# Kernel tuning notes

Hardware: AMD Instinct MI355X
Metric: run time of the kernel (lower is better)

The kernel has to match this reference:

```python
import jax, jax.numpy as jnp
import numpy as np

B, L, DIN = 2, 4096, 1024
W = 64            # windowsize
G, H = 8, 8       # groups, heads per group
DQ = DV = 64
FF = 1024
NEG = -1e30


def rmsnorm(x, gamma, d):
    # F.normalize(x, dim=-1) * sqrt(d) * gamma
    n = jnp.sqrt(jnp.sum(x * x, axis=-1, keepdims=True))
    return x / jnp.maximum(n, 1e-12) * (d ** 0.5) * gamma


def setup_inputs() -> dict:
    key = jax.random.key(0)
    ks = jax.random.split(key, 8)
    s = 0.02
    return {
        "x": jax.random.normal(ks[0], (B, L, DIN), jnp.float32),
        "norm_gamma": jnp.ones((DIN,), jnp.float32),
        "Wq_w": jax.random.normal(ks[1], (G * H * DQ, DIN), jnp.float32) * s,
        "Wq_b": jnp.zeros((G * H * DQ,), jnp.float32),
        "Wkv_w": jax.random.normal(ks[2], (G * (DQ + DV), DIN), jnp.float32) * s,
        "Wkv_b": jnp.zeros((G * (DQ + DV),), jnp.float32),
        "wz_gamma1": jnp.ones((G * H * DV,), jnp.float32),
        "W1_w": jax.random.normal(ks[3], (2 * FF, G * H * DV), jnp.float32) * s,
        "W1_b": jnp.zeros((2 * FF,), jnp.float32),
        "wz_gamma2": jnp.ones((2 * FF,), jnp.float32),
        "W2_w": jax.random.normal(ks[4], (FF, 2 * FF), jnp.float32) * s,
        "W2_b": jnp.zeros((FF,), jnp.float32),
    }


def reference(x, norm_gamma, Wq_w, Wq_b, Wkv_w, Wkv_b,
              wz_gamma1, W1_w, W1_b, wz_gamma2, W2_w, W2_b):
    w2, w4 = W // 2, W // 4
    S = 2 * L // W  # number of query chunks (L % W == 0 -> drop_last path)

    xn = rmsnorm(x, norm_gamma, DIN)
    q = xn @ Wq_w.T + Wq_b          # [B, L, G*H*DQ]
    kv = xn @ Wkv_w.T + Wkv_b       # [B, L, G*(DQ+DV)]

    # pad_to_multiple(kv, W, mod=W//2): L % W == 0 -> append W//2 zeros
    kv = jnp.pad(kv, ((0, 0), (0, w2), (0, 0)))
    k, v = jnp.split(kv, 2, axis=-1)  # each [B, L+W/2, G*DQ]
    # F.pad W//4 both sides, then overlapping windows of size W, stride W//2
    k = jnp.pad(k, ((0, 0), (w4, w4), (0, 0)))  # [B, L+W, G*DQ]
    v = jnp.pad(v, ((0, 0), (w4, w4), (0, 0)))
    idx = jnp.arange(S)[:, None] * w2 + jnp.arange(W)[None, :]  # [S, W] (drop_last applied)
    kwin = k[:, idx].reshape(B, S, W, G, DQ).transpose(0, 3, 1, 2, 4)  # [B,G,S,W,DQ]
    vwin = v[:, idx].reshape(B, S, W, G, DV).transpose(0, 3, 1, 2, 4)  # [B,G,S,W,DV]

    # 'B (S w) (G H D) -> B G H S w D'
    qh = q.reshape(B, S, w2, G, H, DQ).transpose(0, 3, 4, 1, 2, 5)  # [B,G,H,S,w2,DQ]

    qk = jnp.einsum('bghsqd,bgskd->bghsqk', qh, kwin) * (1.0 / DQ ** 0.5)
    # edge masking: first chunk can't see left pad, last chunk can't see right pad
    maskb = jnp.zeros((S, W), bool).at[0, :w4].set(True).at[S - 1, W - w4:].set(True)
    qk = jnp.where(maskb[None, None, None, :, None, :], NEG, qk)
    attn = jax.nn.softmax(qk, axis=-1)
    o = jnp.einsum('bghsqk,bgskd->bghsqd', attn, vwin)
    o = o.transpose(0, 3, 4, 1, 2, 5).reshape(B, L, G * H * DV)  # 'B G H S w D -> B (S w) (G H D)'

    # Wz: RMSNorm -> Linear -> SiLU -> RMSNorm -> Linear -> SiLU (dropout=0)
    z = rmsnorm(o, wz_gamma1, G * H * DV)
    z = jax.nn.silu(z @ W1_w.T + W1_b)
    z = rmsnorm(z, wz_gamma2, 2 * FF)
    z = jax.nn.silu(z @ W2_w.T + W2_b)
    return z
```

## Files before the change

### kernel.cpp

```cpp
#include <hip/hip_runtime.h>
#include <cstdint>

typedef _Float16 f16;
typedef f16 f16x4 __attribute__((ext_vector_type(4)));
typedef f16 f16x8 __attribute__((ext_vector_type(8)));
typedef float f32x4 __attribute__((ext_vector_type(4)));

#define MFMA16(a, b, c) __builtin_amdgcn_mfma_f32_16x16x32_f16(a, b, c, 0, 0, 0)

static __device__ __forceinline__ void gload16(const void* g, void* l) {
    __builtin_amdgcn_global_load_lds(
        (const __attribute__((address_space(1))) uint32_t*)g,
        (__attribute__((address_space(3))) uint32_t*)l, 16, 0, 0);
}

template <int NM, int ND, int NV>
static __device__ __forceinline__ void sgb_phase() {
    if (NV > 0) __builtin_amdgcn_sched_group_barrier(0x10, NV, 0);
    constexpr int PER = NM / ND;
#pragma unroll
    for (int i = 0; i < ND; ++i) {
        __builtin_amdgcn_sched_group_barrier(0x8, PER, 0);
        __builtin_amdgcn_sched_group_barrier(0x100, 1, 0);
    }
    if (NM - PER * ND > 0)
        __builtin_amdgcn_sched_group_barrier(0x8, NM - PER * ND, 0);
}

static __device__ __forceinline__ float blockReduceSum256(float v) {
    __shared__ float red[4];
#pragma unroll
    for (int off = 32; off > 0; off >>= 1) v += __shfl_xor(v, off);
    if ((threadIdx.x & 63) == 0) red[threadIdx.x >> 6] = v;
    __syncthreads();
    return red[0] + red[1] + red[2] + red[3];
}

template <int D>
__global__ __launch_bounds__(256) void k_rowss(const f16* __restrict__ in,
                                               float* __restrict__ sc) {
    constexpr int PER = D / 256;
    size_t row = blockIdx.x;
    const f16* ir = in + row * D;
    int c0 = threadIdx.x * PER;
    float ss = 0.f;
#pragma unroll
    for (int i = 0; i < PER; i += 8) {
        f16x8 h = *reinterpret_cast<const f16x8*>(ir + c0 + i);
#pragma unroll
        for (int e = 0; e < 8; ++e) { float f = (float)h[e]; ss += f * f; }
    }
    ss = blockReduceSum256(ss);
    if (threadIdx.x == 0) sc[row] = ss;
}

__global__ __launch_bounds__(256) void k_prep(
    const float* __restrict__ x, const float* __restrict__ ng, f16* __restrict__ xn,
    const float* __restrict__ Wq_w, const float* __restrict__ Wkv_w,
    const float* __restrict__ W1_w, const float* __restrict__ g1,
    const float* __restrict__ W2_w, const float* __restrict__ g2,
    const float* __restrict__ Wq_b, const float* __restrict__ Wkv_b,
    f16* __restrict__ wqkv, f16* __restrict__ w1, f16* __restrict__ w2,
    float* __restrict__ cb, float* __restrict__ scz) {
    if (blockIdx.x < 8192) {
        size_t row = blockIdx.x;
        const float4 v = reinterpret_cast<const float4*>(x + row * 1024)[threadIdx.x];
        float ss = v.x * v.x + v.y * v.y + v.z * v.z + v.w * v.w;
        ss = blockReduceSum256(ss);
        float sc = 32.0f / fmaxf(sqrtf(ss), 1e-12f);
        const float4 g = reinterpret_cast<const float4*>(ng)[threadIdx.x];
        f16x4 o;
        o[0] = (f16)(v.x * sc * g.x); o[1] = (f16)(v.y * sc * g.y);
        o[2] = (f16)(v.z * sc * g.z); o[3] = (f16)(v.w * sc * g.w);
        *reinterpret_cast<f16x4*>(xn + row * 1024 + threadIdx.x * 4) = o;
        return;
    }
    int i = (blockIdx.x - 8192) * 256 + threadIdx.x;
    if (i < 1048576) {
        float4 v = reinterpret_cast<const float4*>(Wq_w)[i];
        f16x4 o; o[0] = (f16)v.x; o[1] = (f16)v.y; o[2] = (f16)v.z; o[3] = (f16)v.w;
        *reinterpret_cast<f16x4*>(wqkv + (size_t)i * 4) = o;
    } else if (i < 1310720) {
        int j = i - 1048576;
        float4 v = reinterpret_cast<const float4*>(Wkv_w)[j];
        f16x4 o; o[0] = (f16)v.x; o[1] = (f16)v.y; o[2] = (f16)v.z; o[3] = (f16)v.w;
        *reinterpret_cast<f16x4*>(wqkv + 4194304 + (size_t)j * 4) = o;
    } else if (i < 3407872) {
        int j = i - 1310720;
        float4 v = reinterpret_cast<const float4*>(W1_w)[j];
        int c = (j * 4) & 4095;
        f16x4 o;
        o[0] = (f16)(v.x * g1[c]);     o[1] = (f16)(v.y * g1[c + 1]);
        o[2] = (f16)(v.z * g1[c + 2]); o[3] = (f16)(v.w * g1[c + 3]);
        *reinterpret_cast<f16x4*>(w1 + (size_t)j * 4) = o;
    } else if (i < 3932160) {
        int j = i - 3407872;
        float4 v = reinterpret_cast<const float4*>(W2_w)[j];
        int c = (j * 4) & 2047;
        f16x4 o;
        o[0] = (f16)(v.x * g2[c]);     o[1] = (f16)(v.y * g2[c + 1]);
        o[2] = (f16)(v.z * g2[c + 2]); o[3] = (f16)(v.w * g2[c + 3]);
        *reinterpret_cast<f16x4*>(w2 + (size_t)j * 4) = o;
    } else if (i < 3933440) {
        int j = i - 3932160;
        int e = j * 4;
        float4 o4 = (e < 4096) ? reinterpret_cast<const float4*>(Wq_b)[j]
                               : reinterpret_cast<const float4*>(Wkv_b)[(e - 4096) >> 2];
        reinterpret_cast<float4*>(cb)[j] = o4;
    } else if (i < 3937536) {
        int j = i - 3933440;
        reinterpret_cast<float4*>(scz)[j] = make_float4(0.f, 0.f, 0.f, 0.f);
    }
}

template <int BM, int BN, int EPI>
__global__ __launch_bounds__(512, 2) void k_gemm8p(const f16* __restrict__ A,
                                                   const f16* __restrict__ Bt,
                                                   const float* __restrict__ bias,
                                                   const float* __restrict__ ssin,
                                                   float sqrtD,
                                                   void* __restrict__ Cout,
                                                   int M, int N, int K) {
    constexpr int WN = BN / 64, WM = 8 / WN, WR = BM / WM;
    constexpr int MW = WR / 16, MH = MW / 2;
    constexpr int LA = BM / 128, LB = BN / 128;
    constexpr int VS = 2 * LA + LB;
    constexpr int AK = BM * 32;
    constexpr int BKE = BN * 32;
    constexpr int SE = 2 * AK + 2 * BKE;

    __shared__ alignas(16) f16 lds[2 * SE];

    const int mb = M / BM;
    const int cpx = mb >> 3;
    const int xcd = blockIdx.x & 7;
    const int j = blockIdx.x >> 3;
    const int bm = xcd * cpx + (j % cpx);
    const int bn = j / cpx;

    const int tid = threadIdx.x, w = tid >> 6, l = tid & 63;
    const int wm = w / WN, wn = w % WN;
    const int lrow = l & 15, lq = l >> 4;
    const int g = (lrow >> 1) & 3;

    const f16* Ab = A + (size_t)bm * BM * K;
    const f16* Bb = Bt + (size_t)bn * BN * K;
    const int NT = K >> 6;

    int aoff[MW], boff[4];
#pragma unroll
    for (int m = 0; m < MW; ++m)
        aoff[m] = (wm * WR + m * 16 + lrow) * 32 + 8 * (lq ^ g);
#pragma unroll
    for (int n = 0; n < 4; ++n)
        boff[n] = (wn * 64 + n * 16 + lrow) * 32 + 8 * (lq ^ g);

    auto stageA = [&](int k0, f16* region) {
#pragma unroll
        for (int q = 0; q < LA; ++q) {
            int r = q * 128 + w * 16 + (l >> 2);
            int c = 8 * ((l & 3) ^ ((r >> 1) & 3));
            gload16(Ab + (size_t)r * K + k0 + c, region + q * 4096 + w * 512);
        }
    };
    auto stageB = [&](int k0, f16* region) {
#pragma unroll
        for (int q = 0; q < LB; ++q) {
            int r = q * 128 + w * 16 + (l >> 2);
            int c = 8 * ((l & 3) ^ ((r >> 1) & 3));
            gload16(Bb + (size_t)r * K + k0 + c, region + q * 4096 + w * 512);
        }
    };
    auto rdA = [&](f16x8 (&d)[MH], const f16* base, int h) {
#pragma unroll
        for (int m = 0; m < MH; ++m)
            d[m] = *reinterpret_cast<const f16x8*>(base + aoff[h * MH + m]);
    };
    auto rdB = [&](f16x8 (&d)[4], const f16* base) {
#pragma unroll
        for (int n = 0; n < 4; ++n)
            d[n] = *reinterpret_cast<const f16x8*>(base + boff[n]);
    };

    f32x4 acc[MW][4] = {};
    f16x8 afA[MH], afB[MH], bfA[4], bfB[4];

    auto mfmaLo = [&](f16x8 (&af)[MH], f16x8 (&bf)[4]) {
        __builtin_amdgcn_s_setprio(1);
#pragma unroll
        for (int m = 0; m < MH; ++m)
#pragma unroll
            for (int n = 0; n < 4; ++n)
                acc[m][n] = MFMA16(af[m], bf[n], acc[m][n]);
        __builtin_amdgcn_s_setprio(0);
    };
    auto mfmaHi = [&](f16x8 (&af)[MH], f16x8 (&bf)[4]) {
        __builtin_amdgcn_s_setprio(1);
#pragma unroll
        for (int m = 0; m < MH; ++m)
#pragma unroll
            for (int n = 0; n < 4; ++n)
                acc[MH + m][n] = MFMA16(af[m], bf[n], acc[MH + m][n]);
        __builtin_amdgcn_s_setprio(0);
    };

    stageA(0, lds);             stageB(0, lds + 2 * AK);
    stageA(32, lds + AK);       stageB(32, lds + 2 * AK + BKE);
    stageA(64, lds + SE);       stageB(64, lds + SE + 2 * AK);
    asm volatile("s_waitcnt vmcnt(%0)" :: "i"(2 * (LA + LB)) : "memory");
    __builtin_amdgcn_s_barrier();
    rdA(afA, lds, 0);
    rdB(bfA, lds + 2 * AK);

    const int NTm2 = NT - 2;
    for (int t = 0; t < NTm2; ++t) {
        f16* s0 = lds + (t & 1) * SE;
        f16* s1 = lds + ((t & 1) ^ 1) * SE;
        const int kn1 = (t + 1) << 6;
        const int kn2 = (t + 2) << 6;
        __builtin_amdgcn_s_barrier();
        stageA(kn1 + 32, s1 + AK);
        rdA(afB, s0, 1);
        mfmaLo(afA, bfA);
        sgb_phase<MH * 4, MH, LA>();
        asm volatile("s_waitcnt vmcnt(%0)" :: "i"(VS) : "memory");
        __builtin_amdgcn_s_barrier();
        stageB(kn1 + 32, s1 + 2 * AK + BKE);
        rdA(afA, s0 + AK, 0);
        rdB(bfB, s0 + 2 * AK + BKE);
        mfmaHi(afB, bfA);
        sgb_phase<MH * 4, MH + 4, LB>();
        __builtin_amdgcn_s_barrier();
        stageA(kn2, s0);
        rdA(afB, s0 + AK, 1);
        mfmaLo(afA, bfB);
        sgb_phase<MH * 4, MH, LA>();
        asm volatile("s_waitcnt vmcnt(%0)" :: "i"(VS) : "memory");
        __builtin_amdgcn_s_barrier();
        stageB(kn2, s0 + 2 * AK);
        rdA(afA, s1, 0);
        rdB(bfA, s1 + 2 * AK);
        mfmaHi(afB, bfB);
        sgb_phase<MH * 4, MH + 4, LB>();
    }
    {
        const int t = NTm2;
        f16* s0 = lds + (t & 1) * SE;
        f16* s1 = lds + ((t & 1) ^ 1) * SE;
        const int kn1 = (t + 1) << 6;
        __builtin_amdgcn_s_barrier();
        stageA(kn1 + 32, s1 + AK);
        rdA(afB, s0, 1);
        mfmaLo(afA, bfA);
        sgb_phase<MH * 4, MH, LA>();
        asm volatile("s_waitcnt vmcnt(%0)" :: "i"(VS) : "memory");
        __builtin_amdgcn_s_barrier();
        stageB(kn1 + 32, s1 + 2 * AK + BKE);
        rdA(afA, s0 + AK, 0);
        rdB(bfB, s0 + 2 * AK + BKE);
        mfmaHi(afB, bfA);
        sgb_phase<MH * 4, MH + 4, LB>();
        __builtin_amdgcn_s_barrier();
        rdA(afB, s0 + AK, 1);
        mfmaLo(afA, bfB);
        sgb_phase<MH * 4, MH, 0>();
        asm volatile("s_waitcnt vmcnt(%0)" :: "i"(LA + LB) : "memory");
        __builtin_amdgcn_s_barrier();
        rdA(afA, s1, 0);
        rdB(bfA, s1 + 2 * AK);
        mfmaHi(afB, bfB);
        sgb_phase<MH * 4, MH + 4, 0>();
    }
    {
        f16* s0 = lds + ((NT - 1) & 1) * SE;
        __builtin_amdgcn_s_barrier();
        rdA(afB, s0, 1);
        mfmaLo(afA, bfA);
        sgb_phase<MH * 4, MH, 0>();
        asm volatile("s_waitcnt vmcnt(0)" ::: "memory");
        __builtin_amdgcn_s_barrier();
        rdA(afA, s0 + AK, 0);
        rdB(bfB, s0 + 2 * AK + BKE);
        mfmaHi(afB, bfA);
        sgb_phase<MH * 4, MH + 4, 0>();
        __builtin_amdgcn_s_barrier();
        rdA(afB, s0 + AK, 1);
        mfmaLo(afA, bfB);
        sgb_phase<MH * 4, MH, 0>();
        mfmaHi(afB, bfB);
    }

    const size_t row0 = (size_t)bm * BM + wm * WR;
    const int col0 = bn * BN + wn * 64;
    float bsv[4];
#pragma unroll
    for (int n = 0; n < 4; ++n) bsv[n] = bias[col0 + n * 16 + lrow];
#pragma unroll
    for (int m = 0; m < MW; ++m) {
#pragma unroll
        for (int r = 0; r < 4; ++r) {
            const size_t row = row0 + m * 16 + lq * 4 + r;
            float scl = 1.0f;
            if (EPI >= 1) scl = sqrtD * rsqrtf(fmaxf(ssin[row], 1e-24f));
#pragma unroll
            for (int n = 0; n < 4; ++n) {
                float v = acc[m][n][r];
                if (EPI >= 1) v = v * scl;
                v += bsv[n];
                if (EPI >= 1) v = v / (1.f + __expf(-v));
                const size_t idx = row * (size_t)N + col0 + n * 16 + lrow;
                if (EPI == 2) reinterpret_cast<float*>(Cout)[idx] = v;
                else          reinterpret_cast<f16*>(Cout)[idx] = (f16)v;
            }
        }
    }
}

__global__ __launch_bounds__(256) void k_attn(const f16* __restrict__ qkv,
                                              f16* __restrict__ o,
                                              float* __restrict__ ssout) {
    __shared__ alignas(16) f16 Ksm[64 * 64];
    __shared__ alignas(16) f16 Vtsm[64 * 64];
    __shared__ alignas(16) f16 Psm[4][64 * 64];
    const int idx = blockIdx.x;
    const int s = idx & 127;
    const int g = (idx >> 7) & 7;
    const int b = idx >> 10;
    const int tid = threadIdx.x;
    const int w = tid >> 6, l = tid & 63;

    const int baseR = s * 32 - 16;
#pragma unroll
    for (int i = 0; i < 2; ++i) {
        const int j = i * 32 + (tid >> 3);
        const int d0 = (tid & 7) * 8;
        const int R = baseR + j;
        f16x8 kvv = {}, vvv = {};
        if (R >= 0 && R < 4096) {
            const f16* rp = qkv + ((size_t)(b * 4096 + R)) * 5120 + 4096 + g * 64 + d0;
            kvv = *reinterpret_cast<const f16x8*>(rp);
            vvv = *reinterpret_cast<const f16x8*>(rp + 512);
        }
        *reinterpret_cast<f16x8*>(&Ksm[j * 64 + d0]) = kvv;
#pragma unroll
        for (int e = 0; e < 8; ++e) Vtsm[(d0 + e) * 64 + j] = vvv[e];
    }

    const int lrow = l & 15, lk = (l >> 4) * 8;
    f16x8 aq[4][2];
#pragma unroll
    for (int m = 0; m < 4; ++m) {
        const int qr = w * 64 + m * 16 + lrow;
        const int h = qr >> 5, qi = qr & 31;
        const f16* qp = qkv + ((size_t)(b * 4096 + s * 32 + qi)) * 5120 + (g * 8 + h) * 64 + lk;
        aq[m][0] = *reinterpret_cast<const f16x8*>(qp);
        aq[m][1] = *reinterpret_cast<const f16x8*>(qp + 32);
    }
    __syncthreads();

    f32x4 acc[4][4] = {};
#pragma unroll
    for (int kk = 0; kk < 2; ++kk) {
        f16x8 bk[4];
#pragma unroll
        for (int n = 0; n < 4; ++n)
            bk[n] = *reinterpret_cast<const f16x8*>(&Ksm[(n * 16 + lrow) * 64 + kk * 32 + lk]);
#pragma unroll
        for (int m = 0; m < 4; ++m)
#pragma unroll
            for (int n = 0; n < 4; ++n)
                acc[m][n] = MFMA16(aq[m][kk], bk[n], acc[m][n]);
    }

    const int nlo = (s == 0) ? 1 : 0;
    const int nhi = (s == 127) ? 3 : 4;
#pragma unroll
    for (int m = 0; m < 4; ++m) {
#pragma unroll
        for (int r = 0; r < 4; ++r) {
            float xv[4];
#pragma unroll
            for (int n = 0; n < 4; ++n) xv[n] = acc[m][n][r] * 0.125f;
            float mx = -1e30f;
            for (int n = nlo; n < nhi; ++n) mx = fmaxf(mx, xv[n]);
#pragma unroll
            for (int off = 8; off > 0; off >>= 1) mx = fmaxf(mx, __shfl_xor(mx, off));
            float pv[4]; float sum = 0.f;
#pragma unroll
            for (int n = 0; n < 4; ++n) {
                float e = (n >= nlo && n < nhi) ? __expf(xv[n] - mx) : 0.f;
                pv[n] = e; sum += e;
            }
#pragma unroll
            for (int off = 8; off > 0; off >>= 1) sum += __shfl_xor(sum, off);
            const float inv = 1.f / sum;
            const int prow = m * 16 + (l >> 4) * 4 + r;
#pragma unroll
            for (int n = 0; n < 4; ++n)
                Psm[w][prow * 64 + n * 16 + lrow] = (f16)(pv[n] * inv);
        }
    }
    __syncthreads();

    f32x4 oacc[4][4] = {};
#pragma unroll
    for (int kk = 0; kk < 2; ++kk) {
        f16x8 ap[4], bv[4];
#pragma unroll
        for (int m = 0; m < 4; ++m)
            ap[m] = *reinterpret_cast<const f16x8*>(&Psm[w][(m * 16 + lrow) * 64 + kk * 32 + lk]);
#pragma unroll
        for (int n = 0; n < 4; ++n)
            bv[n] = *reinterpret_cast<const f16x8*>(&Vtsm[(n * 16 + lrow) * 64 + kk * 32 + lk]);
#pragma unroll
        for (int m = 0; m < 4; ++m)
#pragma unroll
            for (int n = 0; n < 4; ++n)
                oacc[m][n] = MFMA16(ap[m], bv[n], oacc[m][n]);
    }
    const int lr4 = (l >> 4) * 4;
#pragma unroll
    for (int m = 0; m < 4; ++m) {
#pragma unroll
        for (int r = 0; r < 4; ++r) {
            const int qr = w * 64 + m * 16 + lr4 + r;
            const int h = qr >> 5, qi = qr & 31;
            f16* op = o + ((size_t)(b * 4096 + s * 32 + qi)) * 4096 + (g * 8 + h) * 64;
            float ssp = 0.f;
#pragma unroll
            for (int n = 0; n < 4; ++n) {
                float v = oacc[m][n][r];
                op[n * 16 + lrow] = (f16)v;
                ssp += v * v;
            }
            ssp += __shfl_xor(ssp, 1);
            ssp += __shfl_xor(ssp, 2);
            ssp += __shfl_xor(ssp, 4);
            ssp += __shfl_xor(ssp, 8);
            if (lrow == 0)
                atomicAdd(&ssout[(size_t)(b * 4096 + s * 32 + qi)], ssp);
        }
    }
}

extern "C" void kernel_launch(void* const* d_in, const int* in_sizes, int n_in,
                              void* d_out, int out_size, void* d_ws, size_t ws_size,
                              hipStream_t stream) {
    const float* x     = (const float*)d_in[0];
    const float* ng    = (const float*)d_in[1];
    const float* Wq_w  = (const float*)d_in[2];
    const float* Wq_b  = (const float*)d_in[3];
    const float* Wkv_w = (const float*)d_in[4];
    const float* Wkv_b = (const float*)d_in[5];
    const float* g1    = (const float*)d_in[6];
    const float* W1_w  = (const float*)d_in[7];
    const float* W1_b  = (const float*)d_in[8];
    const float* g2    = (const float*)d_in[9];
    const float* W2_w  = (const float*)d_in[10];
    const float* W2_b  = (const float*)d_in[11];
    float* out = (float*)d_out;

    char* p = (char*)d_ws;
    f16* qkv  = (f16*)(p);
    f16* h1   = (f16*)(p);
    f16* xn   = (f16*)(p + 83886080);
    f16* ob   = (f16*)(p + 83886080);
    f16* w1   = (f16*)(p + 150994944);
    f16* w2   = (f16*)(p + 167772160);
    f16* wqkv = (f16*)(p + 171966464);
    float* cb  = (float*)(p + 182452224);
    float* sc1 = (float*)(p + 182472704);
    float* sc2 = (float*)(p + 182505472);

    k_prep<<<8192 + 15381, 256, 0, stream>>>(x, ng, xn,
                                             Wq_w, Wkv_w, W1_w, g1, W2_w, g2,
                                             Wq_b, Wkv_b, wqkv, w1, w2, cb, sc1);

    k_gemm8p<128, 256, 0><<<1280, 512, 0, stream>>>(xn, wqkv, cb, nullptr, 0.f,
                                                    qkv, 8192, 5120, 1024);

    k_attn<<<2048, 256, 0, stream>>>(qkv, ob, sc1);

    k_gemm8p<256, 256, 1><<<256, 512, 0, stream>>>(ob, w1, W1_b, sc1, 64.0f,
                                                   h1, 8192, 2048, 4096);
    k_rowss<2048><<<8192, 256, 0, stream>>>(h1, sc2);
    k_gemm8p<256, 128, 2><<<256, 512, 0, stream>>>(h1, w2, W2_b, sc2, 45.254834f,
                                                   (void*)out, 8192, 1024, 2048);

    (void)in_sizes; (void)n_in; (void)out_size; (void)ws_size;
}
```

Measured before the change: 354.9 us.

## Restructure GEMM pipeline to BK=32 double-buffered slots with higher occupancy

Replaces the 64-wide K-step, split A/B staging GEMM with a simpler BK=32 two-slot double buffer. Each slot holds combined A and B tiles, so LDS per block shrinks and launch bounds are raised to 4 blocks per CU. Scheduling hints are reorganised to interleave global loads and LDS reads with MFMAs, and s_setprio is dropped. Tile shapes are retuned per GEMM, giving more blocks for the W1 and W2 GEMMs and larger tiles for the QKV projection, at the cost of more barriers per K and register pressure under the tighter occupancy bound.

```diff
diff --git a/kernel.cpp b/kernel.cpp
--- a/kernel.cpp
+++ b/kernel.cpp
@@ -14,17 +14,29 @@
         (__attribute__((address_space(3))) uint32_t*)l, 16, 0, 0);
 }
 
-template <int NM, int ND, int NV>
-static __device__ __forceinline__ void sgb_phase() {
-    if (NV > 0) __builtin_amdgcn_sched_group_barrier(0x10, NV, 0);
-    constexpr int PER = NM / ND;
-#pragma unroll
-    for (int i = 0; i < ND; ++i) {
-        __builtin_amdgcn_sched_group_barrier(0x8, PER, 0);
+template <int NM, int NV>
+static __device__ __forceinline__ void sgb_vm() {
+    constexpr int PER = NM / (NV > 0 ? NV : 1);
+#pragma unroll
+    for (int i = 0; i < NV; ++i) {
+        __builtin_amdgcn_sched_group_barrier(0x10, 1, 0);
+        if (PER > 0) __builtin_amdgcn_sched_group_barrier(0x8, PER, 0);
+    }
+    if (NM - PER * NV > 0)
+        __builtin_amdgcn_sched_group_barrier(0x8, NM - PER * NV, 0);
+}
+template <int NM, int ND>
+static __device__ __forceinline__ void sgb_ds() {
+    constexpr int G = (NM < ND) ? NM : ND;
+    constexpr int PER = (G > 0) ? NM / G : 0;
+#pragma unroll
+    for (int i = 0; i < G; ++i) {
+        if (PER > 0) __builtin_amdgcn_sched_group_barrier(0x8, PER, 0);
         __builtin_amdgcn_sched_group_barrier(0x100, 1, 0);
     }
-    if (NM - PER * ND > 0)
-        __builtin_amdgcn_sched_group_barrier(0x8, NM - PER * ND, 0);
+    if (ND - G > 0) __builtin_amdgcn_sched_group_barrier(0x100, ND - G, 0);
+    if (NM - PER * G > 0)
+        __builtin_amdgcn_sched_group_barrier(0x8, NM - PER * G, 0);
 }
 
 static __device__ __forceinline__ float blockReduceSum256(float v) {
@@ -114,22 +126,20 @@
 }
 
 template <int BM, int BN, int EPI>
-__global__ __launch_bounds__(512, 2) void k_gemm8p(const f16* __restrict__ A,
-                                                   const f16* __restrict__ Bt,
-                                                   const float* __restrict__ bias,
-                                                   const float* __restrict__ ssin,
-                                                   float sqrtD,
-                                                   void* __restrict__ Cout,
-                                                   int M, int N, int K) {
+__global__ __launch_bounds__(512, 4) void k_gemm32k(const f16* __restrict__ A,
+                                                    const f16* __restrict__ Bt,
+                                                    const float* __restrict__ bias,
+                                                    const float* __restrict__ ssin,
+                                                    float sqrtD,
+                                                    void* __restrict__ Cout,
+                                                    int M, int N, int K) {
     constexpr int WN = BN / 64, WM = 8 / WN, WR = BM / WM;
     constexpr int MW = WR / 16, MH = MW / 2;
     constexpr int LA = BM / 128, LB = BN / 128;
-    constexpr int VS = 2 * LA + LB;
-    constexpr int AK = BM * 32;
-    constexpr int BKE = BN * 32;
-    constexpr int SE = 2 * AK + 2 * BKE;
-
-    __shared__ alignas(16) f16 lds[2 * SE];
+    constexpr int LT = LA + LB;
+    constexpr int SA = BM * 32, SB = BN * 32, SLOT = SA + SB;
+
+    __shared__ alignas(16) f16 lds[2 * SLOT];
 
     const int mb = M / BM;
     const int cpx = mb >> 3;
@@ -145,7 +155,7 @@
 
     const f16* Ab = A + (size_t)bm * BM * K;
     const f16* Bb = Bt + (size_t)bn * BN * K;
-    const int NT = K >> 6;
+    const int NT = K >> 5;
 
     int aoff[MW], boff[4];
 #pragma unroll
@@ -153,141 +163,93 @@
         aoff[m] = (wm * WR + m * 16 + lrow) * 32 + 8 * (lq ^ g);
 #pragma unroll
     for (int n = 0; n < 4; ++n)
-        boff[n] = (wn * 64 + n * 16 + lrow) * 32 + 8 * (lq ^ g);
-
-    auto stageA = [&](int k0, f16* region) {
+        boff[n] = SA + (wn * 64 + n * 16 + lrow) * 32 + 8 * (lq ^ g);
+
+    auto stage = [&](int t, f16* slot) {
+        const int k0 = t << 5;
 #pragma unroll
         for (int q = 0; q < LA; ++q) {
             int r = q * 128 + w * 16 + (l >> 2);
             int c = 8 * ((l & 3) ^ ((r >> 1) & 3));
-            gload16(Ab + (size_t)r * K + k0 + c, region + q * 4096 + w * 512);
-        }
-    };
-    auto stageB = [&](int k0, f16* region) {
+            gload16(Ab + (size_t)r * K + k0 + c, slot + q * 4096 + w * 512);
+        }
 #pragma unroll
         for (int q = 0; q < LB; ++q) {
             int r = q * 128 + w * 16 + (l >> 2);
             int c = 8 * ((l & 3) ^ ((r >> 1) & 3));
-            gload16(Bb + (size_t)r * K + k0 + c, region + q * 4096 + w * 512);
+            gload16(Bb + (size_t)r * K + k0 + c, slot + SA + q * 4096 + w * 512);
         }
     };
-    auto rdA = [&](f16x8 (&d)[MH], const f16* base, int h) {
+    auto rdA = [&](f16x8 (&d)[MH], const f16* slot, int h) {
 #pragma unroll
         for (int m = 0; m < MH; ++m)
-            d[m] = *reinterpret_cast<const f16x8*>(base + aoff[h * MH + m]);
+            d[m] = *reinterpret_cast<const f16x8*>(slot + aoff[h * MH + m]);
     };
-    auto rdB = [&](f16x8 (&d)[4], const f16* base) {
+    auto rdB = [&](f16x8 (&d)[4], const f16* slot) {
 #pragma unroll
         for (int n = 0; n < 4; ++n)
-            d[n] = *reinterpret_cast<const f16x8*>(base + boff[n]);
+            d[n] = *reinterpret_cast<const f16x8*>(slot + boff[n]);
     };
 
     f32x4 acc[MW][4] = {};
-    f16x8 afA[MH], afB[MH], bfA[4], bfB[4];
-
-    auto mfmaLo = [&](f16x8 (&af)[MH], f16x8 (&bf)[4]) {
-        __builtin_amdgcn_s_setprio(1);
+    f16x8 afA[MH], afB[MH], bfA[4];
+
+    auto mfmaLo = [&]() {
 #pragma unroll
         for (int m = 0; m < MH; ++m)
 #pragma unroll
             for (int n = 0; n < 4; ++n)
-                acc[m][n] = MFMA16(af[m], bf[n], acc[m][n]);
-        __builtin_amdgcn_s_setprio(0);
+                acc[m][n] = MFMA16(afA[m], bfA[n], acc[m][n]);
     };
-    auto mfmaHi = [&](f16x8 (&af)[MH], f16x8 (&bf)[4]) {
-        __builtin_amdgcn_s_setprio(1);
+    auto mfmaHi = [&]() {
 #pragma unroll
         for (int m = 0; m < MH; ++m)
 #pragma unroll
             for (int n = 0; n < 4; ++n)
-                acc[MH + m][n] = MFMA16(af[m], bf[n], acc[MH + m][n]);
-        __builtin_amdgcn_s_setprio(0);
+                acc[MH + m][n] = MFMA16(afB[m], bfA[n], acc[MH + m][n]);
     };
 
-    stageA(0, lds);             stageB(0, lds + 2 * AK);
-    stageA(32, lds + AK);       stageB(32, lds + 2 * AK + BKE);
-    stageA(64, lds + SE);       stageB(64, lds + SE + 2 * AK);
-    asm volatile("s_waitcnt vmcnt(%0)" :: "i"(2 * (LA + LB)) : "memory");
+    stage(0, lds);
+    stage(1, lds + SLOT);
+    asm volatile("s_waitcnt vmcnt(%0)" :: "i"(LT) : "memory");
     __builtin_amdgcn_s_barrier();
     rdA(afA, lds, 0);
-    rdB(bfA, lds + 2 * AK);
-
-    const int NTm2 = NT - 2;
-    for (int t = 0; t < NTm2; ++t) {
-        f16* s0 = lds + (t & 1) * SE;
-        f16* s1 = lds + ((t & 1) ^ 1) * SE;
-        const int kn1 = (t + 1) << 6;
-        const int kn2 = (t + 2) << 6;
+    rdB(bfA, lds);
+
+    for (int t = 0; t < NT - 2; ++t) {
+        f16* sc_ = lds + (t & 1) * SLOT;
+        f16* sn_ = lds + ((t & 1) ^ 1) * SLOT;
+        rdA(afB, sc_, 1);
+        mfmaLo();
+        sgb_ds<4 * MH, 2 * MH + 4>();
         __builtin_amdgcn_s_barrier();
-        stageA(kn1 + 32, s1 + AK);
-        rdA(afB, s0, 1);
-        mfmaLo(afA, bfA);
-        sgb_phase<MH * 4, MH, LA>();
-        asm volatile("s_waitcnt vmcnt(%0)" :: "i"(VS) : "memory");
+        stage(t + 2, sc_);
+        mfmaHi();
+        sgb_vm<4 * MH, LT>();
+        asm volatile("s_waitcnt vmcnt(%0)" :: "i"(LT) : "memory");
         __builtin_amdgcn_s_barrier();
-        stageB(kn1 + 32, s1 + 2 * AK + BKE);
-        rdA(afA, s0 + AK, 0);
-        rdB(bfB, s0 + 2 * AK + BKE);
-        mfmaHi(afB, bfA);
-        sgb_phase<MH * 4, MH + 4, LB>();
+        rdA(afA, sn_, 0);
+        rdB(bfA, sn_);
+    }
+    {
+        f16* sc_ = lds + ((NT - 2) & 1) * SLOT;
+        f16* sn_ = lds + ((NT - 1) & 1) * SLOT;
+        rdA(afB, sc_, 1);
+        mfmaLo();
+        sgb_ds<4 * MH, 2 * MH + 4>();
         __builtin_amdgcn_s_barrier();
-        stageA(kn2, s0);
-        rdA(afB, s0 + AK, 1);
-        mfmaLo(afA, bfB);
-        sgb_phase<MH * 4, MH, LA>();
-        asm volatile("s_waitcnt vmcnt(%0)" :: "i"(VS) : "memory");
-        __builtin_amdgcn_s_barrier();
-        stageB(kn2, s0 + 2 * AK);
-        rdA(afA, s1, 0);
-        rdB(bfA, s1 + 2 * AK);
-        mfmaHi(afB, bfB);
-        sgb_phase<MH * 4, MH + 4, LB>();
-    }
-    {
-        const int t = NTm2;
-        f16* s0 = lds + (t & 1) * SE;
-        f16* s1 = lds + ((t & 1) ^ 1) * SE;
-        const int kn1 = (t + 1) << 6;
-        __builtin_amdgcn_s_barrier();
-        stageA(kn1 + 32, s1 + AK);
-        rdA(afB, s0, 1);
-        mfmaLo(afA, bfA);
-        sgb_phase<MH * 4, MH, LA>();
-        asm volatile("s_waitcnt vmcnt(%0)" :: "i"(VS) : "memory");
-        __builtin_amdgcn_s_barrier();
-        stageB(kn1 + 32, s1 + 2 * AK + BKE);
-        rdA(afA, s0 + AK, 0);
-        rdB(bfB, s0 + 2 * AK + BKE);
-        mfmaHi(afB, bfA);
-        sgb_phase<MH * 4, MH + 4, LB>();
-        __builtin_amdgcn_s_barrier();
-        rdA(afB, s0 + AK, 1);
-        mfmaLo(afA, bfB);
-        sgb_phase<MH * 4, MH, 0>();
-        asm volatile("s_waitcnt vmcnt(%0)" :: "i"(LA + LB) : "memory");
-        __builtin_amdgcn_s_barrier();
-        rdA(afA, s1, 0);
-        rdB(bfA, s1 + 2 * AK);
-        mfmaHi(afB, bfB);
-        sgb_phase<MH * 4, MH + 4, 0>();
-    }
-    {
-        f16* s0 = lds + ((NT - 1) & 1) * SE;
-        __builtin_amdgcn_s_barrier();
-        rdA(afB, s0, 1);
-        mfmaLo(afA, bfA);
-        sgb_phase<MH * 4, MH, 0>();
+        mfmaHi();
         asm volatile("s_waitcnt vmcnt(0)" ::: "memory");
         __builtin_amdgcn_s_barrier();
-        rdA(afA, s0 + AK, 0);
-        rdB(bfB, s0 + 2 * AK + BKE);
-        mfmaHi(afB, bfA);
-        sgb_phase<MH * 4, MH + 4, 0>();
-        __builtin_amdgcn_s_barrier();
-        rdA(afB, s0 + AK, 1);
-        mfmaLo(afA, bfB);
-        sgb_phase<MH * 4, MH, 0>();
-        mfmaHi(afB, bfB);
+        rdA(afA, sn_, 0);
+        rdB(bfA, sn_);
+    }
+    {
+        f16* sc_ = lds + ((NT - 1) & 1) * SLOT;
+        rdA(afB, sc_, 1);
+        mfmaLo();
+        sgb_ds<4 * MH, 2 * MH + 4>();
+        mfmaHi();
     }
 
     const size_t row0 = (size_t)bm * BM + wm * WR;
@@ -476,16 +438,16 @@
                                              Wq_w, Wkv_w, W1_w, g1, W2_w, g2,
                                              Wq_b, Wkv_b, wqkv, w1, w2, cb, sc1);
 
-    k_gemm8p<128, 256, 0><<<1280, 512, 0, stream>>>(xn, wqkv, cb, nullptr, 0.f,
+    k_gemm32k<256, 256, 0><<<640, 512, 0, stream>>>(xn, wqkv, cb, nullptr, 0.f,
                                                     qkv, 8192, 5120, 1024);
 
     k_attn<<<2048, 256, 0, stream>>>(qkv, ob, sc1);
 
-    k_gemm8p<256, 256, 1><<<256, 512, 0, stream>>>(ob, w1, W1_b, sc1, 64.0f,
-                                                   h1, 8192, 2048, 4096);
+    k_gemm32k<256, 128, 1><<<512, 512, 0, stream>>>(ob, w1, W1_b, sc1, 64.0f,
+                                                    h1, 8192, 2048, 4096);
     k_rowss<2048><<<8192, 256, 0, stream>>>(h1, sc2);
-    k_gemm8p<256, 128, 2><<<256, 512, 0, stream>>>(h1, w2, W2_b, sc2, 45.254834f,
-                                                   (void*)out, 8192, 1024, 2048);
+    k_gemm32k<128, 128, 2><<<512, 512, 0, stream>>>(h1, w2, W2_b, sc2, 45.254834f,
+                                                    (void*)out, 8192, 1024, 2048);
 
     (void)in_sizes; (void)n_in; (void)out_size; (void)ws_size;
 }
```

Result: slower. 1.201 ms (+238.6%).
